# Kernel tuning notes

Measured on AMD Instinct MI355X. Metric: run time of the kernel, lower is better.

The kernel has to match this reference:

```python
import jax, jax.numpy as jnp
import numpy as np

E = 256          # embedding_dim
IN = E + 1       # input feature dim (embedding_dim + 1)
B = 128          # batch
N = 1027         # nodes: 1 source + 1024 candidates + 1 destination + 1 depot
REWIRE_P = 0.1


def setup_inputs() -> dict:
    key = jax.random.key(0)
    ks = jax.random.split(key, 16)
    scale = 1.0 / np.sqrt(IN)

    def lin_w(k):
        return jax.random.normal(k, (E, IN), dtype=jnp.float32) * scale

    def lin_b(k):
        return jax.random.normal(k, (E,), dtype=jnp.float32) * scale

    # sparse small-world rewiring weights: nc scalar writes -> one scatter
    nc = int(IN * E * REWIRE_P)  # 6579
    rows = jax.random.randint(ks[10], (nc,), 0, E)
    cols = jax.random.randint(ks[11], (nc,), 0, IN)
    vals = jax.random.normal(ks[12], (nc,), dtype=jnp.float32) * 0.01
    W_rand = jnp.zeros((E, IN), dtype=jnp.float32).at[rows, cols].set(vals)

    return {
        "solutions": jax.random.normal(ks[0], (B, N, IN), dtype=jnp.float32),
        "W_src": lin_w(ks[1]), "b_src": lin_b(ks[2]),
        "W_dst": lin_w(ks[3]), "b_dst": lin_b(ks[4]),
        "W_dep": lin_w(ks[5]), "b_dep": lin_b(ks[6]),
        "W_cand": lin_w(ks[7]), "b_cand": lin_b(ks[8]),
        "W_reg": lin_w(ks[9]), "b_reg": lin_b(ks[13]),
        "W_rand": W_rand,
        "integration_weight": jnp.float32(0.3),
    }


def reference(solutions, W_src, b_src, W_dst, b_dst, W_dep, b_dep,
              W_cand, b_cand, W_reg, b_reg, W_rand, integration_weight):
    # slice node groups: [B,1,IN], [B,N-3,IN], [B,1,IN], [B,1,IN]
    src = solutions[:, :1, :]
    cand = solutions[:, 1:-2, :]
    dst = solutions[:, -2:-1, :]
    dep = solutions[:, -1:, :]

    def lin(x, W, b):
        return jnp.einsum('bnd,ed->bne', x, W) + b

    def sw(x):
        # SmallWorldLayer: regular linear + 0.1 * sparse random matmul
        return lin(x, W_reg, b_reg) + 0.1 * jnp.einsum('bnd,ed->bne', x, W_rand)

    alpha = jax.nn.sigmoid(integration_weight)

    def mix(emb, sw_out):
        return (1.0 - alpha) * emb + alpha * sw_out

    source_emb = mix(lin(src, W_src, b_src), sw(src))
    candidates_emb = mix(lin(cand, W_cand, b_cand), sw(cand))
    destination_emb = mix(lin(dst, W_dst, b_dst), sw(dst))
    depot_emb = mix(lin(dep, W_dep, b_dep), sw(dep))
    return (source_emb, candidates_emb, destination_emb, depot_emb)
```

## Files before the change

### kernel.cpp

```cpp
#include <hip/hip_runtime.h>
#include <hip/hip_bf16.h>

typedef __bf16 bf16x8 __attribute__((ext_vector_type(8)));
typedef __bf16 bf16x4 __attribute__((ext_vector_type(4)));
typedef float  f32x4  __attribute__((ext_vector_type(4)));
typedef float  f32x4u __attribute__((ext_vector_type(4), aligned(4)));

#define BATCH 128
#define NSOL  1027
#define IND   257
#define EMB   256
#define OUT_SRC  0ULL
#define OUT_CAND 32768ULL
#define OUT_DST  33587200ULL
#define OUT_DEP  33619968ULL

#define WFRAG_OFF 0
#define BEFF_OFF  524288
#define W256_OFF  528384

#define XST_B      528
#define X256_OFF_B 16896
#define BUF_B      17024

__global__ __launch_bounds__(256) void swne_prep(
    const float* __restrict__ Wsrc, const float* __restrict__ bsrc,
    const float* __restrict__ Wdst, const float* __restrict__ bdst,
    const float* __restrict__ Wdep, const float* __restrict__ bdep,
    const float* __restrict__ Wcand, const float* __restrict__ bcand,
    const float* __restrict__ Wreg, const float* __restrict__ breg,
    const float* __restrict__ Wrand, const float* __restrict__ iw,
    char* __restrict__ ws)
{
    const float a  = 1.0f / (1.0f + expf(-iw[0]));
    const float ca = 1.0f - a;
    const float sa = 0.1f * a;

    const float* Ws[4] = {Wsrc, Wcand, Wdst, Wdep};
    const float* Bs[4] = {bsrc, bcand, bdst, bdep};

    const int gid = blockIdx.x * 256 + threadIdx.x;
    const int gsz = gridDim.x * 256;

    float* beff = (float*)(ws + BEFF_OFF);
    float* w256 = (float*)(ws + W256_OFF);
    for (int i = gid; i < 4 * EMB; i += gsz) {
        int seg = i >> 8, e = i & 255;
        beff[i] = ca * Bs[seg][e] + a * breg[e];
        int si = e * IND + 256;
        w256[i] = ca * Ws[seg][si] + a * Wreg[si] + sa * Wrand[si];
    }

    __bf16* wfr = (__bf16*)(ws + WFRAG_OFF);
    for (int i = gid; i < 4 * 65536; i += gsz) {
        int seg  = i >> 16;
        int rem  = i & 65535;
        int kk   = rem >> 13;
        int rem2 = rem & 8191;
        int cg   = rem2 >> 9;
        int rem3 = rem2 & 511;
        int l    = rem3 >> 3;
        int j    = rem3 & 7;
        int e = cg * 16 + (l & 15);
        int k = kk * 32 + (l >> 4) * 8 + j;
        int si = e * IND + k;
        wfr[i] = (__bf16)(ca * Ws[seg][si] + a * Wreg[si] + sa * Wrand[si]);
    }
}

#define BARRIER() { asm volatile("s_waitcnt lgkmcnt(0)" ::: "memory"); \
  __builtin_amdgcn_s_barrier(); asm volatile("" ::: "memory"); }

#define ISSUE(xb, xstr, pf, pf256) { \
  _Pragma("unroll") for (int rr = 0; rr < 4; ++rr) \
    pf[rr] = *((const f32x4u*)((xb) + (size_t)(wave * 4 + rr) * (xstr)) + lane); \
  if (tid < 32) pf256 = (xb)[(size_t)tid * (xstr) + 256]; }

#define WRITEB(boff, pf, pf256) { \
  _Pragma("unroll") for (int rr = 0; rr < 4; ++rr) { \
    const int r_ = wave * 4 + rr; \
    bf16x4 h_; \
    h_[0] = (__bf16)pf[rr][0]; h_[1] = (__bf16)pf[rr][1]; \
    h_[2] = (__bf16)pf[rr][2]; h_[3] = (__bf16)pf[rr][3]; \
    *(bf16x4*)(smem + (boff) + r_ * XST_B + lane * 8) = h_; } \
  if (tid < 32) *(float*)(smem + (boff) + X256_OFF_B + tid * 4) = pf256; }

#define COMPSTORE(boff, obase, W, B4, W4) { \
  f32x4 acc[2][2]; \
  _Pragma("unroll") for (int rt = 0; rt < 2; ++rt) \
    _Pragma("unroll") for (int n = 0; n < 2; ++n) { f32x4 z_ = {0.f,0.f,0.f,0.f}; acc[rt][n] = z_; } \
  _Pragma("unroll") for (int kk = 0; kk < 8; ++kk) { \
    bf16x8 a0 = *(const bf16x8*)(smem + (boff) + rl * XST_B + kk * 64 + grp * 16); \
    bf16x8 a1 = *(const bf16x8*)(smem + (boff) + (16 + rl) * XST_B + kk * 64 + grp * 16); \
    _Pragma("unroll") for (int n = 0; n < 2; ++n) { \
      acc[0][n] = __builtin_amdgcn_mfma_f32_16x16x32_bf16(W[kk][n], a0, acc[0][n], 0, 0, 0); \
      acc[1][n] = __builtin_amdgcn_mfma_f32_16x16x32_bf16(W[kk][n], a1, acc[1][n], 0, 0, 0); } } \
  _Pragma("unroll") for (int rt = 0; rt < 2; ++rt) { \
    const float xl = *(const float*)(smem + (boff) + X256_OFF_B + (rt * 16 + rl) * 4); \
    float* op_ = (obase) + (size_t)(rt * 16 + rl) * 256 + wave * 32 + grp * 4; \
    _Pragma("unroll") for (int n = 0; n < 2; ++n) { \
      f32x4 r_ = acc[rt][n] + xl * W4[n] + B4[n]; \
      __builtin_nontemporal_store(r_, (f32x4*)(op_ + n * 16)); } } }

__device__ __forceinline__ const float* cand_x(const float* sol, int T) {
    const int bb = T >> 5, t = T & 31;
    return sol + ((size_t)bb * NSOL + 1 + t * 32) * IND;
}
__device__ __forceinline__ float* cand_o(float* out, int T) {
    const int bb = T >> 5, t = T & 31;
    return out + OUT_CAND + ((size_t)bb * 1024 + t * 32) * 256;
}

__global__ __launch_bounds__(512, 2) void swne_main(const float* __restrict__ sol,
                                                    const char* __restrict__ ws,
                                                    float* __restrict__ out)
{
    __shared__ __align__(16) char smem[4 * BUF_B];
    const int tid = threadIdx.x, bid = blockIdx.x;
    const int lane = tid & 63, wave = tid >> 6;
    const int rl = lane & 15, grp = lane >> 4;

    const bf16x8* wfb = (const bf16x8*)(ws + WFRAG_OFF);
    f32x4 pfA[4], pfB[4]; float pA256 = 0.f, pB256 = 0.f;

    if (bid < 1024) {
        bf16x8 wreg[8][2];
        #pragma unroll
        for (int kk = 0; kk < 8; ++kk)
            #pragma unroll
            for (int n = 0; n < 2; ++n)
                wreg[kk][n] = wfb[(size_t)(((8 + kk) * 16) + (wave * 2 + n)) * 64 + lane];

        const float* bc = (const float*)(ws + BEFF_OFF) + 256;
        const float* wc = (const float*)(ws + W256_OFF) + 256;
        f32x4 b4[2], w4[2];
        #pragma unroll
        for (int n = 0; n < 2; ++n) {
            b4[n] = *(const f32x4*)(bc + wave * 32 + n * 16 + grp * 4);
            w4[n] = *(const f32x4*)(wc + wave * 32 + n * 16 + grp * 4);
        }

        const int T0 = bid * 4;

        ISSUE(cand_x(sol, T0 + 0), IND, pfA, pA256);
        ISSUE(cand_x(sol, T0 + 1), IND, pfB, pB256);
        WRITEB(0 * BUF_B, pfA, pA256);
        WRITEB(1 * BUF_B, pfB, pB256);
        ISSUE(cand_x(sol, T0 + 2), IND, pfA, pA256);
        ISSUE(cand_x(sol, T0 + 3), IND, pfB, pB256);
        BARRIER();

        COMPSTORE((size_t)0 * BUF_B, cand_o(out, T0 + 0), wreg, b4, w4);
        WRITEB((size_t)2 * BUF_B, pfA, pA256);
        COMPSTORE((size_t)1 * BUF_B, cand_o(out, T0 + 1), wreg, b4, w4);
        WRITEB((size_t)3 * BUF_B, pfB, pB256);
        BARRIER();

        COMPSTORE((size_t)2 * BUF_B, cand_o(out, T0 + 2), wreg, b4, w4);
        COMPSTORE((size_t)3 * BUF_B, cand_o(out, T0 + 3), wreg, b4, w4);
    } else {
        const int e = bid - 1024;
        const int s3 = e >> 2, tt = e & 3;
        const int seg = (s3 == 0) ? 0 : (s3 == 1 ? 2 : 3);
        const int nrow = (s3 == 0) ? 0 : (s3 == 1 ? 1025 : 1026);
        const size_t outb = (s3 == 0) ? OUT_SRC : (s3 == 1 ? OUT_DST : OUT_DEP);
        const float* xe = sol + ((size_t)(tt * 32) * NSOL + nrow) * IND;
        float* oe = out + outb + (size_t)(tt * 32) * 256;
        const size_t xstrE = (size_t)NSOL * IND;

        bf16x8 wregE[8][2];
        #pragma unroll
        for (int kk = 0; kk < 8; ++kk)
            #pragma unroll
            for (int n = 0; n < 2; ++n)
                wregE[kk][n] = wfb[(size_t)(((seg * 8 + kk) * 16) + (wave * 2 + n)) * 64 + lane];
        const float* bcE = (const float*)(ws + BEFF_OFF) + seg * 256;
        const float* wcE = (const float*)(ws + W256_OFF) + seg * 256;
        f32x4 b4E[2], w4E[2];
        #pragma unroll
        for (int n = 0; n < 2; ++n) {
            b4E[n] = *(const f32x4*)(bcE + wave * 32 + n * 16 + grp * 4);
            w4E[n] = *(const f32x4*)(wcE + wave * 32 + n * 16 + grp * 4);
        }

        ISSUE(xe, xstrE, pfA, pA256);
        WRITEB(0, pfA, pA256);
        BARRIER();
        COMPSTORE(0, oe, wregE, b4E, w4E);
    }
}

extern "C" void kernel_launch(void* const* d_in, const int* in_sizes, int n_in,
                              void* d_out, int out_size, void* d_ws, size_t ws_size,
                              hipStream_t stream) {
    const float* sol   = (const float*)d_in[0];
    const float* Wsrc  = (const float*)d_in[1];
    const float* bsrc  = (const float*)d_in[2];
    const float* Wdst  = (const float*)d_in[3];
    const float* bdst  = (const float*)d_in[4];
    const float* Wdep  = (const float*)d_in[5];
    const float* bdep  = (const float*)d_in[6];
    const float* Wcand = (const float*)d_in[7];
    const float* bcand = (const float*)d_in[8];
    const float* Wreg  = (const float*)d_in[9];
    const float* breg  = (const float*)d_in[10];
    const float* Wrand = (const float*)d_in[11];
    const float* iw    = (const float*)d_in[12];

    swne_prep<<<512, 256, 0, stream>>>(Wsrc, bsrc, Wdst, bdst, Wdep, bdep,
                                       Wcand, bcand, Wreg, breg, Wrand, iw,
                                       (char*)d_ws);
    swne_main<<<1036, 512, 0, stream>>>(sol, (const char*)d_ws, (float*)d_out);
}
```

Before: 65.68 us.

## Fuse weight prep into main kernel and process eight tiles per block

Removes the separate prep kernel: each block now builds its combined bf16 weight fragments, bias and last-column weights in registers directly from the fp32 inputs. This drops one launch and the workspace round trip. The candidate blocks now handle eight 32-row tiles instead of four, with a longer software pipeline over the four LDS buffers, so the grid shrinks to 524 blocks. The cost is redundant per-block weight reads and arithmetic from global/L2, and fewer blocks for load balancing.

```diff
diff --git a/kernel.cpp b/kernel.cpp
--- a/kernel.cpp
+++ b/kernel.cpp
@@ -6,67 +6,16 @@
 typedef float  f32x4  __attribute__((ext_vector_type(4)));
 typedef float  f32x4u __attribute__((ext_vector_type(4), aligned(4)));
 
-#define BATCH 128
 #define NSOL  1027
 #define IND   257
-#define EMB   256
 #define OUT_SRC  0ULL
 #define OUT_CAND 32768ULL
 #define OUT_DST  33587200ULL
 #define OUT_DEP  33619968ULL
 
-#define WFRAG_OFF 0
-#define BEFF_OFF  524288
-#define W256_OFF  528384
-
 #define XST_B      528
 #define X256_OFF_B 16896
 #define BUF_B      17024
-
-__global__ __launch_bounds__(256) void swne_prep(
-    const float* __restrict__ Wsrc, const float* __restrict__ bsrc,
-    const float* __restrict__ Wdst, const float* __restrict__ bdst,
-    const float* __restrict__ Wdep, const float* __restrict__ bdep,
-    const float* __restrict__ Wcand, const float* __restrict__ bcand,
-    const float* __restrict__ Wreg, const float* __restrict__ breg,
-    const float* __restrict__ Wrand, const float* __restrict__ iw,
-    char* __restrict__ ws)
-{
-    const float a  = 1.0f / (1.0f + expf(-iw[0]));
-    const float ca = 1.0f - a;
-    const float sa = 0.1f * a;
-
-    const float* Ws[4] = {Wsrc, Wcand, Wdst, Wdep};
-    const float* Bs[4] = {bsrc, bcand, bdst, bdep};
-
-    const int gid = blockIdx.x * 256 + threadIdx.x;
-    const int gsz = gridDim.x * 256;
-
-    float* beff = (float*)(ws + BEFF_OFF);
-    float* w256 = (float*)(ws + W256_OFF);
-    for (int i = gid; i < 4 * EMB; i += gsz) {
-        int seg = i >> 8, e = i & 255;
-        beff[i] = ca * Bs[seg][e] + a * breg[e];
-        int si = e * IND + 256;
-        w256[i] = ca * Ws[seg][si] + a * Wreg[si] + sa * Wrand[si];
-    }
-
-    __bf16* wfr = (__bf16*)(ws + WFRAG_OFF);
-    for (int i = gid; i < 4 * 65536; i += gsz) {
-        int seg  = i >> 16;
-        int rem  = i & 65535;
-        int kk   = rem >> 13;
-        int rem2 = rem & 8191;
-        int cg   = rem2 >> 9;
-        int rem3 = rem2 & 511;
-        int l    = rem3 >> 3;
-        int j    = rem3 & 7;
-        int e = cg * 16 + (l & 15);
-        int k = kk * 32 + (l >> 4) * 8 + j;
-        int si = e * IND + k;
-        wfr[i] = (__bf16)(ca * Ws[seg][si] + a * Wreg[si] + sa * Wrand[si]);
-    }
-}
 
 #define BARRIER() { asm volatile("s_waitcnt lgkmcnt(0)" ::: "memory"); \
   __builtin_amdgcn_s_barrier(); asm volatile("" ::: "memory"); }
@@ -85,7 +34,32 @@
     *(bf16x4*)(smem + (boff) + r_ * XST_B + lane * 8) = h_; } \
   if (tid < 32) *(float*)(smem + (boff) + X256_OFF_B + tid * 4) = pf256; }
 
-#define COMPSTORE(boff, obase, W, B4, W4) { \
+#define BUILD_W() { \
+  _Pragma("unroll") for (int n = 0; n < 2; ++n) { \
+    const int e_ = wave * 32 + n * 16 + rl; \
+    const float* pc_ = Wseg + (size_t)e_ * IND; \
+    const float* pr_ = Wrg  + (size_t)e_ * IND; \
+    const float* pd_ = Wrnd + (size_t)e_ * IND; \
+    _Pragma("unroll") for (int kk = 0; kk < 8; ++kk) { \
+      const int k0_ = kk * 32 + grp * 8; \
+      f32x4 c0 = *(const f32x4u*)(pc_ + k0_), c1 = *(const f32x4u*)(pc_ + k0_ + 4); \
+      f32x4 r0 = *(const f32x4u*)(pr_ + k0_), r1 = *(const f32x4u*)(pr_ + k0_ + 4); \
+      f32x4 d0 = *(const f32x4u*)(pd_ + k0_), d1 = *(const f32x4u*)(pd_ + k0_ + 4); \
+      bf16x8 wv_; \
+      _Pragma("unroll") for (int j = 0; j < 4; ++j) { \
+        wv_[j]     = (__bf16)(ca * c0[j] + a * r0[j] + sa * d0[j]); \
+        wv_[j + 4] = (__bf16)(ca * c1[j] + a * r1[j] + sa * d1[j]); } \
+      wreg[kk][n] = wv_; } } \
+  _Pragma("unroll") for (int n = 0; n < 2; ++n) { \
+    const int e0_ = wave * 32 + n * 16 + grp * 4; \
+    f32x4 bs_ = *(const f32x4u*)(Bseg + e0_); \
+    f32x4 br_ = *(const f32x4u*)(brg + e0_); \
+    _Pragma("unroll") for (int j = 0; j < 4; ++j) { \
+      const size_t si_ = (size_t)(e0_ + j) * IND + 256; \
+      b4[n][j] = ca * bs_[j] + a * br_[j]; \
+      w4[n][j] = ca * Wseg[si_] + a * Wrg[si_] + sa * Wrnd[si_]; } } }
+
+#define COMPSTORE(boff, obase) { \
   f32x4 acc[2][2]; \
   _Pragma("unroll") for (int rt = 0; rt < 2; ++rt) \
     _Pragma("unroll") for (int n = 0; n < 2; ++n) { f32x4 z_ = {0.f,0.f,0.f,0.f}; acc[rt][n] = z_; } \
@@ -93,13 +67,13 @@
     bf16x8 a0 = *(const bf16x8*)(smem + (boff) + rl * XST_B + kk * 64 + grp * 16); \
     bf16x8 a1 = *(const bf16x8*)(smem + (boff) + (16 + rl) * XST_B + kk * 64 + grp * 16); \
     _Pragma("unroll") for (int n = 0; n < 2; ++n) { \
-      acc[0][n] = __builtin_amdgcn_mfma_f32_16x16x32_bf16(W[kk][n], a0, acc[0][n], 0, 0, 0); \
-      acc[1][n] = __builtin_amdgcn_mfma_f32_16x16x32_bf16(W[kk][n], a1, acc[1][n], 0, 0, 0); } } \
+      acc[0][n] = __builtin_amdgcn_mfma_f32_16x16x32_bf16(wreg[kk][n], a0, acc[0][n], 0, 0, 0); \
+      acc[1][n] = __builtin_amdgcn_mfma_f32_16x16x32_bf16(wreg[kk][n], a1, acc[1][n], 0, 0, 0); } } \
   _Pragma("unroll") for (int rt = 0; rt < 2; ++rt) { \
     const float xl = *(const float*)(smem + (boff) + X256_OFF_B + (rt * 16 + rl) * 4); \
     float* op_ = (obase) + (size_t)(rt * 16 + rl) * 256 + wave * 32 + grp * 4; \
     _Pragma("unroll") for (int n = 0; n < 2; ++n) { \
-      f32x4 r_ = acc[rt][n] + xl * W4[n] + B4[n]; \
+      f32x4 r_ = acc[rt][n] + xl * w4[n] + b4[n]; \
       __builtin_nontemporal_store(r_, (f32x4*)(op_ + n * 16)); } } }
 
 __device__ __forceinline__ const float* cand_x(const float* sol, int T) {
@@ -111,83 +85,87 @@
     return out + OUT_CAND + ((size_t)bb * 1024 + t * 32) * 256;
 }
 
-__global__ __launch_bounds__(512, 2) void swne_main(const float* __restrict__ sol,
-                                                    const char* __restrict__ ws,
-                                                    float* __restrict__ out)
+__global__ __launch_bounds__(512, 2) void swne_fused(
+    const float* __restrict__ sol,
+    const float* __restrict__ Wsrc, const float* __restrict__ bsrc,
+    const float* __restrict__ Wdst, const float* __restrict__ bdst,
+    const float* __restrict__ Wdep, const float* __restrict__ bdep,
+    const float* __restrict__ Wcand, const float* __restrict__ bcand,
+    const float* __restrict__ Wrg, const float* __restrict__ brg,
+    const float* __restrict__ Wrnd, const float* __restrict__ iw,
+    float* __restrict__ out)
 {
     __shared__ __align__(16) char smem[4 * BUF_B];
     const int tid = threadIdx.x, bid = blockIdx.x;
     const int lane = tid & 63, wave = tid >> 6;
     const int rl = lane & 15, grp = lane >> 4;
 
-    const bf16x8* wfb = (const bf16x8*)(ws + WFRAG_OFF);
-    f32x4 pfA[4], pfB[4]; float pA256 = 0.f, pB256 = 0.f;
+    const float a  = 1.0f / (1.0f + expf(-iw[0]));
+    const float ca = 1.0f - a;
+    const float sa = 0.1f * a;
 
-    if (bid < 1024) {
-        bf16x8 wreg[8][2];
-        #pragma unroll
-        for (int kk = 0; kk < 8; ++kk)
-            #pragma unroll
-            for (int n = 0; n < 2; ++n)
-                wreg[kk][n] = wfb[(size_t)(((8 + kk) * 16) + (wave * 2 + n)) * 64 + lane];
+    bf16x8 wreg[8][2];
+    f32x4 b4[2], w4[2];
+    f32x4 pfA[4], pfB[4];
+    float pA256 = 0.f, pB256 = 0.f;
 
-        const float* bc = (const float*)(ws + BEFF_OFF) + 256;
-        const float* wc = (const float*)(ws + W256_OFF) + 256;
-        f32x4 b4[2], w4[2];
-        #pragma unroll
-        for (int n = 0; n < 2; ++n) {
-            b4[n] = *(const f32x4*)(bc + wave * 32 + n * 16 + grp * 4);
-            w4[n] = *(const f32x4*)(wc + wave * 32 + n * 16 + grp * 4);
-        }
-
-        const int T0 = bid * 4;
-
-        ISSUE(cand_x(sol, T0 + 0), IND, pfA, pA256);
-        ISSUE(cand_x(sol, T0 + 1), IND, pfB, pB256);
-        WRITEB(0 * BUF_B, pfA, pA256);
-        WRITEB(1 * BUF_B, pfB, pB256);
-        ISSUE(cand_x(sol, T0 + 2), IND, pfA, pA256);
-        ISSUE(cand_x(sol, T0 + 3), IND, pfB, pB256);
-        BARRIER();
-
-        COMPSTORE((size_t)0 * BUF_B, cand_o(out, T0 + 0), wreg, b4, w4);
-        WRITEB((size_t)2 * BUF_B, pfA, pA256);
-        COMPSTORE((size_t)1 * BUF_B, cand_o(out, T0 + 1), wreg, b4, w4);
-        WRITEB((size_t)3 * BUF_B, pfB, pB256);
-        BARRIER();
-
-        COMPSTORE((size_t)2 * BUF_B, cand_o(out, T0 + 2), wreg, b4, w4);
-        COMPSTORE((size_t)3 * BUF_B, cand_o(out, T0 + 3), wreg, b4, w4);
-    } else {
-        const int e = bid - 1024;
-        const int s3 = e >> 2, tt = e & 3;
-        const int seg = (s3 == 0) ? 0 : (s3 == 1 ? 2 : 3);
+    if (bid < 12) {
+        const int s3 = bid >> 2, tt = bid & 3;
         const int nrow = (s3 == 0) ? 0 : (s3 == 1 ? 1025 : 1026);
         const size_t outb = (s3 == 0) ? OUT_SRC : (s3 == 1 ? OUT_DST : OUT_DEP);
+        const float* Wseg = (s3 == 0) ? Wsrc : (s3 == 1 ? Wdst : Wdep);
+        const float* Bseg = (s3 == 0) ? bsrc : (s3 == 1 ? bdst : bdep);
         const float* xe = sol + ((size_t)(tt * 32) * NSOL + nrow) * IND;
         float* oe = out + outb + (size_t)(tt * 32) * 256;
         const size_t xstrE = (size_t)NSOL * IND;
 
-        bf16x8 wregE[8][2];
-        #pragma unroll
-        for (int kk = 0; kk < 8; ++kk)
-            #pragma unroll
-            for (int n = 0; n < 2; ++n)
-                wregE[kk][n] = wfb[(size_t)(((seg * 8 + kk) * 16) + (wave * 2 + n)) * 64 + lane];
-        const float* bcE = (const float*)(ws + BEFF_OFF) + seg * 256;
-        const float* wcE = (const float*)(ws + W256_OFF) + seg * 256;
-        f32x4 b4E[2], w4E[2];
-        #pragma unroll
-        for (int n = 0; n < 2; ++n) {
-            b4E[n] = *(const f32x4*)(bcE + wave * 32 + n * 16 + grp * 4);
-            w4E[n] = *(const f32x4*)(wcE + wave * 32 + n * 16 + grp * 4);
-        }
-
         ISSUE(xe, xstrE, pfA, pA256);
+        BUILD_W();
         WRITEB(0, pfA, pA256);
         BARRIER();
-        COMPSTORE(0, oe, wregE, b4E, w4E);
+        COMPSTORE(0, oe);
+        return;
     }
+
+    const float* Wseg = Wcand;
+    const float* Bseg = bcand;
+    const int T0 = (bid - 12) * 8;
+
+    ISSUE(cand_x(sol, T0 + 0), IND, pfA, pA256);
+    ISSUE(cand_x(sol, T0 + 1), IND, pfB, pB256);
+
+    BUILD_W();
+
+    WRITEB(0 * BUF_B, pfA, pA256);
+    WRITEB(1 * BUF_B, pfB, pB256);
+    ISSUE(cand_x(sol, T0 + 2), IND, pfA, pA256);
+    ISSUE(cand_x(sol, T0 + 3), IND, pfB, pB256);
+    BARRIER();
+
+    COMPSTORE((size_t)0 * BUF_B, cand_o(out, T0 + 0));
+    WRITEB((size_t)2 * BUF_B, pfA, pA256);
+    ISSUE(cand_x(sol, T0 + 4), IND, pfA, pA256);
+    COMPSTORE((size_t)1 * BUF_B, cand_o(out, T0 + 1));
+    WRITEB((size_t)3 * BUF_B, pfB, pB256);
+    ISSUE(cand_x(sol, T0 + 5), IND, pfB, pB256);
+    BARRIER();
+
+    COMPSTORE((size_t)2 * BUF_B, cand_o(out, T0 + 2));
+    WRITEB((size_t)0 * BUF_B, pfA, pA256);
+    ISSUE(cand_x(sol, T0 + 6), IND, pfA, pA256);
+    COMPSTORE((size_t)3 * BUF_B, cand_o(out, T0 + 3));
+    WRITEB((size_t)1 * BUF_B, pfB, pB256);
+    ISSUE(cand_x(sol, T0 + 7), IND, pfB, pB256);
+    BARRIER();
+
+    COMPSTORE((size_t)0 * BUF_B, cand_o(out, T0 + 4));
+    WRITEB((size_t)2 * BUF_B, pfA, pA256);
+    COMPSTORE((size_t)1 * BUF_B, cand_o(out, T0 + 5));
+    WRITEB((size_t)3 * BUF_B, pfB, pB256);
+    BARRIER();
+
+    COMPSTORE((size_t)2 * BUF_B, cand_o(out, T0 + 6));
+    COMPSTORE((size_t)3 * BUF_B, cand_o(out, T0 + 7));
 }
 
 extern "C" void kernel_launch(void* const* d_in, const int* in_sizes, int n_in,
@@ -207,8 +185,7 @@
     const float* Wrand = (const float*)d_in[11];
     const float* iw    = (const float*)d_in[12];
 
-    swne_prep<<<512, 256, 0, stream>>>(Wsrc, bsrc, Wdst, bdst, Wdep, bdep,
-                                       Wcand, bcand, Wreg, breg, Wrand, iw,
-                                       (char*)d_ws);
-    swne_main<<<1036, 512, 0, stream>>>(sol, (const char*)d_ws, (float*)d_out);
+    swne_fused<<<524, 512, 0, stream>>>(sol, Wsrc, bsrc, Wdst, bdst, Wdep, bdep,
+                                        Wcand, bcand, Wreg, breg, Wrand, iw,
+                                        (float*)d_out);
 }
```

Measured after the change: 225.2 us. 243% more time.
